# Performance work log

Measured on AMD Instinct MI355X. Metric: run time of the kernel, lower is better.

## Reference

```python
import jax, jax.numpy as jnp
import numpy as np

B, C, H, W = 8, 512, 64, 64
DEPTH, HEADS = 4, 8


def setup_inputs() -> dict:
    key = jax.random.key(0)
    ks = jax.random.split(key, 7)
    s = 0.02
    return {
        "x": jax.random.normal(ks[0], (B, C, H, W), jnp.float32),
        # axial positional embeddings, emb dim at index 1: (1,C,H,1) and (1,C,1,W)
        "pos_h": jax.random.normal(ks[1], (C, H), jnp.float32) * s,
        "pos_w": jax.random.normal(ks[2], (C, W), jnp.float32) * s,
        # per layer, per axis (0=height, 1=width): q, kv, out projections
        "wq": jax.random.normal(ks[3], (DEPTH, 2, C, C), jnp.float32) * s,
        "wkv": jax.random.normal(ks[4], (DEPTH, 2, C, 2 * C), jnp.float32) * s,
        "wo": jax.random.normal(ks[5], (DEPTH, 2, C, C), jnp.float32) * s,
        "wo_b": jax.random.normal(ks[6], (DEPTH, 2, C), jnp.float32) * s,
    }


def _attn_last_axis(x, wq, wkv, wo, wo_b, heads):
    """Self-attention along the second-to-last axis. x: (..., L, C)."""
    lead = x.shape[:-2]
    L, Cd = x.shape[-2], x.shape[-1]
    e = Cd // heads
    q = x @ wq                       # (..., L, C)
    k, v = jnp.split(x @ wkv, 2, axis=-1)
    sh = lead + (L, heads, e)
    q, k, v = q.reshape(sh), k.reshape(sh), v.reshape(sh)
    dots = jnp.einsum('...ihe,...jhe->...hij', q, k) * (e ** -0.5)
    attn = jax.nn.softmax(dots, axis=-1)
    out = jnp.einsum('...hij,...jhe->...ihe', attn, v).reshape(lead + (L, heads * e))
    return out @ wo + wo_b


def reference(x, pos_h, pos_w, wq, wkv, wo, wo_b):
    # positional embedding: x + (1,C,H,1) + (1,C,1,W)
    x = x + pos_h[None, :, :, None] + pos_w[None, :, None, :]
    y = jnp.transpose(x, (0, 2, 3, 1))  # (B,H,W,C) channels-last working layout
    for l in range(DEPTH):
        # height-axis attention: (B,W,H,C), attend along H
        yh = jnp.transpose(y, (0, 2, 1, 3))
        oh = _attn_last_axis(yh, wq[l, 0], wkv[l, 0], wo[l, 0], wo_b[l, 0], HEADS)
        oh = jnp.transpose(oh, (0, 2, 1, 3))
        # width-axis attention: attend along W
        ow = _attn_last_axis(y, wq[l, 1], wkv[l, 1], wo[l, 1], wo_b[l, 1], HEADS)
        y = oh + ow  # sum_axial_out=True, no residual
    return jnp.transpose(y, (0, 3, 1, 2))  # back to (B,C,H,W)
```

## Files before the change

kernel.cpp:

```cpp
#include <hip/hip_runtime.h>
#include <stdint.h>


typedef __attribute__((ext_vector_type(8))) short bf16x8;
typedef __attribute__((ext_vector_type(4))) float f32x4;
typedef unsigned short u16;
typedef unsigned int u32;

#define MFMA16(a, b, c) __builtin_amdgcn_mfma_f32_16x16x32_bf16((a), (b), (c), 0, 0, 0)

__device__ __forceinline__ float b2f(u16 h) {
    u32 u = ((u32)h) << 16;
    float f;
    __builtin_memcpy(&f, &u, 4);
    return f;
}
__device__ __forceinline__ u16 f2b(float f) {
    u32 u;
    __builtin_memcpy(&u, &f, 4);
    u32 r = (u + 0x7fffu + ((u >> 16) & 1u)) >> 16;
    return (u16)r;
}

#define GLD_LDS16(g, l)                                                        \
    __builtin_amdgcn_global_load_lds(                                          \
        (const __attribute__((address_space(1))) void*)(g),                    \
        (__attribute__((address_space(3))) void*)(l), 16, 0, 0)

__global__ __launch_bounds__(256) void embed_kernel(
    const float* __restrict__ x, const float* __restrict__ ph,
    const float* __restrict__ pw, u16* __restrict__ y)
{
    __shared__ float tile[64][65];
    const int c0 = blockIdx.x * 64, h = blockIdx.y, b = blockIdx.z;
    const int t = threadIdx.x;
#pragma unroll
    for (int i = 0; i < 4; ++i) {
        int cl = (t >> 4) + i * 16;
        int w4 = (t & 15) * 4;
        const float* src = x + (((size_t)(b * 512 + c0 + cl)) * 64 + h) * 64 + w4;
        float4 v = *(const float4*)src;
        float p = ph[(c0 + cl) * 64 + h];
        tile[cl][w4 + 0] = v.x + p + pw[(c0 + cl) * 64 + w4 + 0];
        tile[cl][w4 + 1] = v.y + p + pw[(c0 + cl) * 64 + w4 + 1];
        tile[cl][w4 + 2] = v.z + p + pw[(c0 + cl) * 64 + w4 + 2];
        tile[cl][w4 + 3] = v.w + p + pw[(c0 + cl) * 64 + w4 + 3];
    }
    __syncthreads();
    const int wl = t >> 2, cb = (t & 3) * 16;
    bf16x8 o0, o1;
#pragma unroll
    for (int j = 0; j < 8; ++j) o0[j] = (short)f2b(tile[cb + j][wl]);
#pragma unroll
    for (int j = 0; j < 8; ++j) o1[j] = (short)f2b(tile[cb + 8 + j][wl]);
    u16* dst = y + (((size_t)(b * 64 + h) * 64 + wl) * 512 + c0 + cb);
    *(bf16x8*)dst = o0;
    *(bf16x8*)(dst + 8) = o1;
}

__global__ __launch_bounds__(256) void wtrans_kernel(
    const float* __restrict__ wq, const float* __restrict__ wkv,
    const float* __restrict__ wo, u16* __restrict__ wT)
{
    const int mid = blockIdx.z;
    const int l = mid / 6, rest = mid % 6, axis = rest / 3, which = rest % 3;
    const size_t la = (size_t)(l * 2 + axis);
    const float* src;
    int N;
    size_t doff;
    if (which == 0)      { src = wq  + la * 512 * 512;  N = 512;  doff = la * (2048 * 512); }
    else if (which == 1) { src = wkv + la * 512 * 1024; N = 1024; doff = la * (2048 * 512) + 512 * 512; }
    else                 { src = wo  + la * 512 * 512;  N = 512;  doff = la * (2048 * 512) + 512 * 512 + 1024 * 512; }
    const int n0 = blockIdx.y * 64;
    if (n0 >= N) return;
    const int k0 = blockIdx.x * 64;
    __shared__ float tile[64][65];
    const int t = threadIdx.x;
#pragma unroll
    for (int i = 0; i < 4; ++i) {
        int kl = (t >> 4) + i * 16;
        int n4 = (t & 15) * 4;
        float4 v = *(const float4*)(src + (size_t)(k0 + kl) * N + n0 + n4);
        tile[kl][n4 + 0] = v.x; tile[kl][n4 + 1] = v.y;
        tile[kl][n4 + 2] = v.z; tile[kl][n4 + 3] = v.w;
    }
    __syncthreads();
    const int nl = t >> 2, kb = (t & 3) * 16;
    bf16x8 o0, o1;
#pragma unroll
    for (int j = 0; j < 8; ++j) o0[j] = (short)f2b(tile[kb + j][nl]);
#pragma unroll
    for (int j = 0; j < 8; ++j) o1[j] = (short)f2b(tile[kb + 8 + j][nl]);
    u16* dst = wT + doff + (size_t)(n0 + nl) * 512 + k0 + kb;
    *(bf16x8*)dst = o0;
    *(bf16x8*)(dst + 8) = o1;
}

template <int MODE>
__global__ __launch_bounds__(256) void gemm_bt(
    const u16* __restrict__ A, int lda,
    const u16* __restrict__ Bt,
    const float* __restrict__ bias,
    u16* C, int ldc)
{
    __shared__ u16 As[128 * 64];
    __shared__ u16 Bs[128 * 64];
    const int tid = threadIdx.x;
    const int lane = tid & 63;
    const int wv = tid >> 6;
    const int wr = (wv >> 1) * 64, wc = (wv & 1) * 64;
    const int nbx = gridDim.x;
    int lin = blockIdx.x + nbx * blockIdx.y;
    int cpx = (nbx * gridDim.y) >> 3;
    int id = (lin & 7) * cpx + (lin >> 3);
    const int n0 = (id % nbx) * 128;
    const int m0 = (id / nbx) * 128;
    const int rl = lane >> 3;
    const int cp = lane & 7;
    const int l16 = lane & 15;
    const int g = lane >> 4;
    const int kgrp = g << 3;
    f32x4 acc[4][4] = {};

    for (int ks = 0; ks < 512; ks += 64) {
#pragma unroll
        for (int i = 0; i < 4; ++i) {
            int row = wv * 8 + i * 32 + rl;
            int clog = cp ^ (row & 7);
            const u16* src = A + (size_t)(m0 + row) * lda + ks + clog * 8;
            GLD_LDS16(src, As + (wv * 8 + i * 32) * 64);
        }
#pragma unroll
        for (int i = 0; i < 4; ++i) {
            int row = wv * 8 + i * 32 + rl;
            int clog = cp ^ (row & 7);
            const u16* src = Bt + (size_t)(n0 + row) * 512 + ks + clog * 8;
            GLD_LDS16(src, Bs + (wv * 8 + i * 32) * 64);
        }
        __syncthreads();
#pragma unroll
        for (int kk = 0; kk < 2; ++kk) {
            bf16x8 af[4], bfr[4];
            const int kb = (kk * 32 + kgrp) * 2;
#pragma unroll
            for (int mf = 0; mf < 4; ++mf) {
                int row = wr + mf * 16 + l16;
                af[mf] = *(const bf16x8*)((const char*)As + row * 128 + (kb ^ ((row & 7) << 4)));
            }
#pragma unroll
            for (int nf = 0; nf < 4; ++nf) {
                int row = wc + nf * 16 + l16;
                bfr[nf] = *(const bf16x8*)((const char*)Bs + row * 128 + (kb ^ ((row & 7) << 4)));
            }
#pragma unroll
            for (int nf = 0; nf < 4; ++nf)
#pragma unroll
                for (int mf = 0; mf < 4; ++mf)
                    acc[nf][mf] = MFMA16(bfr[nf], af[mf], acc[nf][mf]);
        }
        __syncthreads();
    }

    float bv[4][4];
    if (MODE >= 1) {
#pragma unroll
        for (int nf = 0; nf < 4; ++nf) {
            float4 b4 = *(const float4*)(bias + n0 + wc + nf * 16 + g * 4);
            bv[nf][0] = b4.x; bv[nf][1] = b4.y; bv[nf][2] = b4.z; bv[nf][3] = b4.w;
        }
    }
#pragma unroll
    for (int mf = 0; mf < 4; ++mf) {
        const int m = m0 + wr + mf * 16 + l16;
#pragma unroll
        for (int nf = 0; nf < 4; ++nf) {
            const int n = n0 + wc + nf * 16 + g * 4;
            u16* cptr = C + (size_t)m * ldc + n;
            float v0 = acc[nf][mf][0], v1 = acc[nf][mf][1];
            float v2 = acc[nf][mf][2], v3 = acc[nf][mf][3];
            if (MODE >= 1) { v0 += bv[nf][0]; v1 += bv[nf][1]; v2 += bv[nf][2]; v3 += bv[nf][3]; }
            if (MODE == 2) {
                ushort4 o = *(const ushort4*)cptr;
                v0 += b2f(o.x); v1 += b2f(o.y); v2 += b2f(o.z); v3 += b2f(o.w);
            }
            uint2 pk;
            pk.x = (u32)f2b(v0) | ((u32)f2b(v1) << 16);
            pk.y = (u32)f2b(v2) | ((u32)f2b(v3) << 16);
            *(uint2*)cptr = pk;
        }
    }
}

__global__ __launch_bounds__(256) void attn_kernel(u16* QKV, int bstr, int tstr)
{
    __shared__ u16 sm[4][2][64 * 64];
    const int bi = blockIdx.x;
    const int base = (bi >> 6) * 4096 + (bi & 63) * bstr;
    const int tid = threadIdx.x, lane = tid & 63, wv = tid >> 6;
    const int l16 = lane & 15, g = lane >> 4;
    const int kgrp = g << 3;
    const int rl = lane >> 3, cp = lane & 7;
    u16* Kl = (u16*)sm[wv][0];
    u16* Vt = (u16*)sm[wv][1];

    for (int hh = 0; hh < 2; ++hh) {
        const int head = wv + hh * 4;
        const int hoff = head * 64;

#pragma unroll
        for (int i = 0; i < 8; ++i) {
            int row = i * 8 + rl;
            int clog = cp ^ (row & 7);
            const u16* src = QKV + (size_t)(base + row * tstr) * 1536 + 512 + hoff + clog * 8;
            GLD_LDS16(src, Kl + i * 8 * 64);
        }
        bf16x8 q[4][2];
#pragma unroll
        for (int i_f = 0; i_f < 4; ++i_f)
#pragma unroll
            for (int k2 = 0; k2 < 2; ++k2)
                q[i_f][k2] = *(const bf16x8*)(QKV + (size_t)(base + (i_f * 16 + l16) * tstr) * 1536
                                              + hoff + k2 * 32 + kgrp);
        bf16x8 vvr[8];
#pragma unroll
        for (int i = 0; i < 8; ++i)
            vvr[i] = *(const bf16x8*)(QKV + (size_t)(base + (i * 8 + rl) * tstr) * 1536
                                      + 1024 + hoff + cp * 8);

        asm volatile("s_waitcnt vmcnt(0)" ::: "memory");
        __builtin_amdgcn_sched_barrier(0);

        f32x4 st[4][4] = {};
#pragma unroll
        for (int k2 = 0; k2 < 2; ++k2) {
            bf16x8 kf[4];
            const int kb = (k2 * 32 + kgrp) * 2;
#pragma unroll
            for (int j_f = 0; j_f < 4; ++j_f) {
                int row = j_f * 16 + l16;
                kf[j_f] = *(const bf16x8*)((const char*)Kl + row * 128 + (kb ^ ((row & 7) << 4)));
            }
#pragma unroll
            for (int i_f = 0; i_f < 4; ++i_f)
#pragma unroll
                for (int j_f = 0; j_f < 4; ++j_f)
                    st[i_f][j_f] = MFMA16(kf[j_f], q[i_f][k2], st[i_f][j_f]);
        }

#pragma unroll
        for (int i = 0; i < 8; ++i) {
            int j2 = i * 16 + rl * 2;
#pragma unroll
            for (int t = 0; t < 8; ++t) {
                int e = cp * 8 + t;
                int addr = e * 128 + (j2 ^ (((t ^ cp) & 7) << 4));
                *(u16*)((char*)Vt + addr) = (u16)vvr[i][t];
            }
        }

#pragma unroll
        for (int i_f = 0; i_f < 4; ++i_f) {
            const int irow = i_f * 16 + l16;
            float ev[4][4];
            float mx = -1e30f;
#pragma unroll
            for (int j_f = 0; j_f < 4; ++j_f)
#pragma unroll
                for (int r = 0; r < 4; ++r) {
                    float v = st[i_f][j_f][r] * 0.125f;
                    ev[j_f][r] = v;
                    mx = fmaxf(mx, v);
                }
            mx = fmaxf(mx, __shfl_xor(mx, 16, 64));
            mx = fmaxf(mx, __shfl_xor(mx, 32, 64));
            float sum = 0.f;
#pragma unroll
            for (int j_f = 0; j_f < 4; ++j_f)
#pragma unroll
                for (int r = 0; r < 4; ++r) {
                    float e = __expf(ev[j_f][r] - mx);
                    ev[j_f][r] = e;
                    sum += e;
                }
            sum += __shfl_xor(sum, 16, 64);
            sum += __shfl_xor(sum, 32, 64);
            float inv = __builtin_amdgcn_rcpf(sum);
#pragma unroll
            for (int j_f = 0; j_f < 4; ++j_f) {
                uint2 pk;
                pk.x = (u32)f2b(ev[j_f][0] * inv) | ((u32)f2b(ev[j_f][1] * inv) << 16);
                pk.y = (u32)f2b(ev[j_f][2] * inv) | ((u32)f2b(ev[j_f][3] * inv) << 16);
                int addr = irow * 128 + ((j_f * 32 + g * 8) ^ ((irow & 7) << 4));
                *(uint2*)((char*)Kl + addr) = pk;
            }
        }

        f32x4 of[4][4] = {};
#pragma unroll
        for (int k2 = 0; k2 < 2; ++k2) {
            bf16x8 vf[4], pf[4];
            const int kb = (k2 * 32 + kgrp) * 2;
#pragma unroll
            for (int e_f = 0; e_f < 4; ++e_f) {
                int row = e_f * 16 + l16;
                int sw = ((row & 7) ^ ((row >> 3) & 7)) << 4;
                vf[e_f] = *(const bf16x8*)((const char*)Vt + row * 128 + (kb ^ sw));
            }
#pragma unroll
            for (int i_f = 0; i_f < 4; ++i_f) {
                int row = i_f * 16 + l16;
                pf[i_f] = *(const bf16x8*)((const char*)Kl + row * 128 + (kb ^ ((row & 7) << 4)));
            }
#pragma unroll
            for (int e_f = 0; e_f < 4; ++e_f)
#pragma unroll
                for (int i_f = 0; i_f < 4; ++i_f)
                    of[e_f][i_f] = MFMA16(vf[e_f], pf[i_f], of[e_f][i_f]);
        }

#pragma unroll
        for (int i_f = 0; i_f < 4; ++i_f) {
            const int i = i_f * 16 + l16;
            u16* orow = QKV + (size_t)(base + i * tstr) * 1536 + hoff + g * 4;
#pragma unroll
            for (int e_f = 0; e_f < 4; ++e_f) {
                uint2 pk;
                pk.x = (u32)f2b(of[e_f][i_f][0]) | ((u32)f2b(of[e_f][i_f][1]) << 16);
                pk.y = (u32)f2b(of[e_f][i_f][2]) | ((u32)f2b(of[e_f][i_f][3]) << 16);
                *(uint2*)(orow + e_f * 16) = pk;
            }
        }
        asm volatile("s_waitcnt lgkmcnt(0)" ::: "memory");
        __builtin_amdgcn_sched_barrier(0);
    }
}

__global__ __launch_bounds__(256) void untrans_kernel(
    const u16* __restrict__ y, float* __restrict__ out)
{
    __shared__ float tile[64][65];
    const int c0 = blockIdx.x * 64, h = blockIdx.y, b = blockIdx.z;
    const int t = threadIdx.x;
    {
        const int wl = t >> 2, cb = (t & 3) * 16;
        const u16* src = y + (((size_t)(b * 64 + h) * 64 + wl) * 512 + c0 + cb);
        bf16x8 v0 = *(const bf16x8*)src;
        bf16x8 v1 = *(const bf16x8*)(src + 8);
#pragma unroll
        for (int j = 0; j < 8; ++j) tile[wl][cb + j] = b2f((u16)v0[j]);
#pragma unroll
        for (int j = 0; j < 8; ++j) tile[wl][cb + 8 + j] = b2f((u16)v1[j]);
    }
    __syncthreads();
    const int cl = t >> 2, w16 = (t & 3) * 16;
    float* dst = out + (((size_t)(b * 512 + c0 + cl)) * 64 + h) * 64 + w16;
#pragma unroll
    for (int j = 0; j < 4; ++j) {
        float4 v;
        v.x = tile[w16 + j * 4 + 0][cl];
        v.y = tile[w16 + j * 4 + 1][cl];
        v.z = tile[w16 + j * 4 + 2][cl];
        v.w = tile[w16 + j * 4 + 3][cl];
        *(float4*)(dst + j * 4) = v;
    }
}

extern "C" void kernel_launch(void* const* d_in, const int* in_sizes, int n_in,
                              void* d_out, int out_size, void* d_ws, size_t ws_size,
                              hipStream_t stream)
{
    (void)in_sizes; (void)n_in; (void)out_size; (void)ws_size;
    const float* x   = (const float*)d_in[0];
    const float* ph  = (const float*)d_in[1];
    const float* pw  = (const float*)d_in[2];
    const float* wq  = (const float*)d_in[3];
    const float* wkv = (const float*)d_in[4];
    const float* wo  = (const float*)d_in[5];
    const float* wob = (const float*)d_in[6];

    char* ws = (char*)d_ws;
    u16* yA  = (u16*)(ws);
    u16* yB  = (u16*)(ws + 33554432);
    u16* QKV = (u16*)(ws + 67108864);
    u16* wT  = (u16*)(ws + 167772160);
    float* out = (float*)d_out;

    embed_kernel<<<dim3(8, 64, 8), 256, 0, stream>>>(x, ph, pw, yA);
    wtrans_kernel<<<dim3(8, 16, 24), 256, 0, stream>>>(wq, wkv, wo, wT);

    u16* yin = yA;
    u16* yout = yB;
    for (int l = 0; l < 4; ++l) {
        for (int axis = 0; axis < 2; ++axis) {
            const u16* wTla = wT + (size_t)(l * 2 + axis) * 2048 * 512;
            const float* bias = wob + (size_t)(l * 2 + axis) * 512;
            gemm_bt<0><<<dim3(12, 256), 256, 0, stream>>>(yin, 512, wTla, nullptr, QKV, 1536);
            int bstr = (axis == 0) ? 1 : 64;
            int tstr = (axis == 0) ? 64 : 1;
            attn_kernel<<<dim3(512), 256, 0, stream>>>(QKV, bstr, tstr);
            const u16* woT = wTla + 512 * 512 + 1024 * 512;
            if (axis == 0)
                gemm_bt<1><<<dim3(4, 256), 256, 0, stream>>>(QKV, 1536, woT, bias, yout, 512);
            else
                gemm_bt<2><<<dim3(4, 256), 256, 0, stream>>>(QKV, 1536, woT, bias, yout, 512);
        }
        u16* tmp = yin; yin = yout; yout = tmp;
    }
    untrans_kernel<<<dim3(8, 64, 8), 256, 0, stream>>>(yin, out);
}
```

Before: 1.233 ms.

## Store height-axis QKV transposed so attention reads contiguous rows, one head per wave

The QKV GEMM epilogue for the height axis now writes rows in permuted order (swapping h and w within each batch), so the attention kernel always reads contiguous sequence rows instead of strided ones. The out-projection GEMM uses the same inverse permutation when writing y. The attention kernel drops its two-head loop and strided addressing, assigning one (sequence, head) unit per wave and doubling the grid. This removes the 64-row stride for height attention and adds occupancy, at the cost of scattered row writes in the GEMM epilogues.

```diff
diff --git a/kernel.cpp b/kernel.cpp
--- a/kernel.cpp
+++ b/kernel.cpp
@@ -96,7 +96,7 @@
     *(bf16x8*)(dst + 8) = o1;
 }
 
-template <int MODE>
+template <int MODE, int PERM>
 __global__ __launch_bounds__(256) void gemm_bt(
     const u16* __restrict__ A, int lda,
     const u16* __restrict__ Bt,
@@ -172,10 +172,12 @@
 #pragma unroll
     for (int mf = 0; mf < 4; ++mf) {
         const int m = m0 + wr + mf * 16 + l16;
+        const int mp = PERM ? ((m & ~4095) | ((m & 63) << 6) | ((m >> 6) & 63)) : m;
+        u16* crow = C + (size_t)mp * ldc;
 #pragma unroll
         for (int nf = 0; nf < 4; ++nf) {
             const int n = n0 + wc + nf * 16 + g * 4;
-            u16* cptr = C + (size_t)m * ldc + n;
+            u16* cptr = crow + n;
             float v0 = acc[nf][mf][0], v1 = acc[nf][mf][1];
             float v2 = acc[nf][mf][2], v3 = acc[nf][mf][3];
             if (MODE >= 1) { v0 += bv[nf][0]; v1 += bv[nf][1]; v2 += bv[nf][2]; v3 += bv[nf][3]; }
@@ -191,147 +193,141 @@
     }
 }
 
-__global__ __launch_bounds__(256) void attn_kernel(u16* QKV, int bstr, int tstr)
+__global__ __launch_bounds__(256) void attn_kernel(u16* QKV)
 {
     __shared__ u16 sm[4][2][64 * 64];
-    const int bi = blockIdx.x;
-    const int base = (bi >> 6) * 4096 + (bi & 63) * bstr;
     const int tid = threadIdx.x, lane = tid & 63, wv = tid >> 6;
+    const int unit = blockIdx.x * 4 + wv;
+    const int base = (unit >> 3) * 64;
+    const int hoff = (unit & 7) * 64;
     const int l16 = lane & 15, g = lane >> 4;
     const int kgrp = g << 3;
     const int rl = lane >> 3, cp = lane & 7;
     u16* Kl = (u16*)sm[wv][0];
     u16* Vt = (u16*)sm[wv][1];
 
-    for (int hh = 0; hh < 2; ++hh) {
-        const int head = wv + hh * 4;
-        const int hoff = head * 64;
-
-#pragma unroll
-        for (int i = 0; i < 8; ++i) {
-            int row = i * 8 + rl;
-            int clog = cp ^ (row & 7);
-            const u16* src = QKV + (size_t)(base + row * tstr) * 1536 + 512 + hoff + clog * 8;
-            GLD_LDS16(src, Kl + i * 8 * 64);
-        }
-        bf16x8 q[4][2];
+#pragma unroll
+    for (int i = 0; i < 8; ++i) {
+        int row = i * 8 + rl;
+        int clog = cp ^ (row & 7);
+        const u16* src = QKV + (size_t)(base + row) * 1536 + 512 + hoff + clog * 8;
+        GLD_LDS16(src, Kl + i * 8 * 64);
+    }
+    bf16x8 q[4][2];
+#pragma unroll
+    for (int i_f = 0; i_f < 4; ++i_f)
+#pragma unroll
+        for (int k2 = 0; k2 < 2; ++k2)
+            q[i_f][k2] = *(const bf16x8*)(QKV + (size_t)(base + i_f * 16 + l16) * 1536
+                                          + hoff + k2 * 32 + kgrp);
+    bf16x8 vvr[8];
+#pragma unroll
+    for (int i = 0; i < 8; ++i)
+        vvr[i] = *(const bf16x8*)(QKV + (size_t)(base + i * 8 + rl) * 1536
+                                  + 1024 + hoff + cp * 8);
+
+    asm volatile("s_waitcnt vmcnt(0)" ::: "memory");
+    __builtin_amdgcn_sched_barrier(0);
+
+    f32x4 st[4][4] = {};
+#pragma unroll
+    for (int k2 = 0; k2 < 2; ++k2) {
+        bf16x8 kf[4];
+        const int kb = (k2 * 32 + kgrp) * 2;
+#pragma unroll
+        for (int j_f = 0; j_f < 4; ++j_f) {
+            int row = j_f * 16 + l16;
+            kf[j_f] = *(const bf16x8*)((const char*)Kl + row * 128 + (kb ^ ((row & 7) << 4)));
+        }
 #pragma unroll
         for (int i_f = 0; i_f < 4; ++i_f)
 #pragma unroll
-            for (int k2 = 0; k2 < 2; ++k2)
-                q[i_f][k2] = *(const bf16x8*)(QKV + (size_t)(base + (i_f * 16 + l16) * tstr) * 1536
-                                              + hoff + k2 * 32 + kgrp);
-        bf16x8 vvr[8];
-#pragma unroll
-        for (int i = 0; i < 8; ++i)
-            vvr[i] = *(const bf16x8*)(QKV + (size_t)(base + (i * 8 + rl) * tstr) * 1536
-                                      + 1024 + hoff + cp * 8);
-
-        asm volatile("s_waitcnt vmcnt(0)" ::: "memory");
-        __builtin_amdgcn_sched_barrier(0);
-
-        f32x4 st[4][4] = {};
-#pragma unroll
-        for (int k2 = 0; k2 < 2; ++k2) {
-            bf16x8 kf[4];
-            const int kb = (k2 * 32 + kgrp) * 2;
-#pragma unroll
-            for (int j_f = 0; j_f < 4; ++j_f) {
-                int row = j_f * 16 + l16;
-                kf[j_f] = *(const bf16x8*)((const char*)Kl + row * 128 + (kb ^ ((row & 7) << 4)));
+            for (int j_f = 0; j_f < 4; ++j_f)
+                st[i_f][j_f] = MFMA16(kf[j_f], q[i_f][k2], st[i_f][j_f]);
+    }
+
+#pragma unroll
+    for (int i = 0; i < 8; ++i) {
+        int j2 = i * 16 + rl * 2;
+#pragma unroll
+        for (int t = 0; t < 8; ++t) {
+            int e = cp * 8 + t;
+            int addr = e * 128 + (j2 ^ (((t ^ cp) & 7) << 4));
+            *(u16*)((char*)Vt + addr) = (u16)vvr[i][t];
+        }
+    }
+
+#pragma unroll
+    for (int i_f = 0; i_f < 4; ++i_f) {
+        const int irow = i_f * 16 + l16;
+        float ev[4][4];
+        float mx = -1e30f;
+#pragma unroll
+        for (int j_f = 0; j_f < 4; ++j_f)
+#pragma unroll
+            for (int r = 0; r < 4; ++r) {
+                float v = st[i_f][j_f][r] * 0.125f;
+                ev[j_f][r] = v;
+                mx = fmaxf(mx, v);
             }
+        mx = fmaxf(mx, __shfl_xor(mx, 16, 64));
+        mx = fmaxf(mx, __shfl_xor(mx, 32, 64));
+        float sum = 0.f;
+#pragma unroll
+        for (int j_f = 0; j_f < 4; ++j_f)
+#pragma unroll
+            for (int r = 0; r < 4; ++r) {
+                float e = __expf(ev[j_f][r] - mx);
+                ev[j_f][r] = e;
+                sum += e;
+            }
+        sum += __shfl_xor(sum, 16, 64);
+        sum += __shfl_xor(sum, 32, 64);
+        float inv = __builtin_amdgcn_rcpf(sum);
+#pragma unroll
+        for (int j_f = 0; j_f < 4; ++j_f) {
+            uint2 pk;
+            pk.x = (u32)f2b(ev[j_f][0] * inv) | ((u32)f2b(ev[j_f][1] * inv) << 16);
+            pk.y = (u32)f2b(ev[j_f][2] * inv) | ((u32)f2b(ev[j_f][3] * inv) << 16);
+            int addr = irow * 128 + ((j_f * 32 + g * 8) ^ ((irow & 7) << 4));
+            *(uint2*)((char*)Kl + addr) = pk;
+        }
+    }
+
+    f32x4 of[4][4] = {};
+#pragma unroll
+    for (int k2 = 0; k2 < 2; ++k2) {
+        bf16x8 vf[4], pf[4];
+        const int kb = (k2 * 32 + kgrp) * 2;
+#pragma unroll
+        for (int e_f = 0; e_f < 4; ++e_f) {
+            int row = e_f * 16 + l16;
+            int sw = ((row & 7) ^ ((row >> 3) & 7)) << 4;
+            vf[e_f] = *(const bf16x8*)((const char*)Vt + row * 128 + (kb ^ sw));
+        }
+#pragma unroll
+        for (int i_f = 0; i_f < 4; ++i_f) {
+            int row = i_f * 16 + l16;
+            pf[i_f] = *(const bf16x8*)((const char*)Kl + row * 128 + (kb ^ ((row & 7) << 4)));
+        }
+#pragma unroll
+        for (int e_f = 0; e_f < 4; ++e_f)
 #pragma unroll
             for (int i_f = 0; i_f < 4; ++i_f)
-#pragma unroll
-                for (int j_f = 0; j_f < 4; ++j_f)
-                    st[i_f][j_f] = MFMA16(kf[j_f], q[i_f][k2], st[i_f][j_f]);
-        }
-
-#pragma unroll
-        for (int i = 0; i < 8; ++i) {
-            int j2 = i * 16 + rl * 2;
-#pragma unroll
-            for (int t = 0; t < 8; ++t) {
-                int e = cp * 8 + t;
-                int addr = e * 128 + (j2 ^ (((t ^ cp) & 7) << 4));
-                *(u16*)((char*)Vt + addr) = (u16)vvr[i][t];
-            }
-        }
-
-#pragma unroll
-        for (int i_f = 0; i_f < 4; ++i_f) {
-            const int irow = i_f * 16 + l16;
-            float ev[4][4];
-            float mx = -1e30f;
-#pragma unroll
-            for (int j_f = 0; j_f < 4; ++j_f)
-#pragma unroll
-                for (int r = 0; r < 4; ++r) {
-                    float v = st[i_f][j_f][r] * 0.125f;
-                    ev[j_f][r] = v;
-                    mx = fmaxf(mx, v);
-                }
-            mx = fmaxf(mx, __shfl_xor(mx, 16, 64));
-            mx = fmaxf(mx, __shfl_xor(mx, 32, 64));
-            float sum = 0.f;
-#pragma unroll
-            for (int j_f = 0; j_f < 4; ++j_f)
-#pragma unroll
-                for (int r = 0; r < 4; ++r) {
-                    float e = __expf(ev[j_f][r] - mx);
-                    ev[j_f][r] = e;
-                    sum += e;
-                }
-            sum += __shfl_xor(sum, 16, 64);
-            sum += __shfl_xor(sum, 32, 64);
-            float inv = __builtin_amdgcn_rcpf(sum);
-#pragma unroll
-            for (int j_f = 0; j_f < 4; ++j_f) {
-                uint2 pk;
-                pk.x = (u32)f2b(ev[j_f][0] * inv) | ((u32)f2b(ev[j_f][1] * inv) << 16);
-                pk.y = (u32)f2b(ev[j_f][2] * inv) | ((u32)f2b(ev[j_f][3] * inv) << 16);
-                int addr = irow * 128 + ((j_f * 32 + g * 8) ^ ((irow & 7) << 4));
-                *(uint2*)((char*)Kl + addr) = pk;
-            }
-        }
-
-        f32x4 of[4][4] = {};
-#pragma unroll
-        for (int k2 = 0; k2 < 2; ++k2) {
-            bf16x8 vf[4], pf[4];
-            const int kb = (k2 * 32 + kgrp) * 2;
-#pragma unroll
-            for (int e_f = 0; e_f < 4; ++e_f) {
-                int row = e_f * 16 + l16;
-                int sw = ((row & 7) ^ ((row >> 3) & 7)) << 4;
-                vf[e_f] = *(const bf16x8*)((const char*)Vt + row * 128 + (kb ^ sw));
-            }
-#pragma unroll
-            for (int i_f = 0; i_f < 4; ++i_f) {
-                int row = i_f * 16 + l16;
-                pf[i_f] = *(const bf16x8*)((const char*)Kl + row * 128 + (kb ^ ((row & 7) << 4)));
-            }
-#pragma unroll
-            for (int e_f = 0; e_f < 4; ++e_f)
-#pragma unroll
-                for (int i_f = 0; i_f < 4; ++i_f)
-                    of[e_f][i_f] = MFMA16(vf[e_f], pf[i_f], of[e_f][i_f]);
-        }
-
-#pragma unroll
-        for (int i_f = 0; i_f < 4; ++i_f) {
-            const int i = i_f * 16 + l16;
-            u16* orow = QKV + (size_t)(base + i * tstr) * 1536 + hoff + g * 4;
-#pragma unroll
-            for (int e_f = 0; e_f < 4; ++e_f) {
-                uint2 pk;
-                pk.x = (u32)f2b(of[e_f][i_f][0]) | ((u32)f2b(of[e_f][i_f][1]) << 16);
-                pk.y = (u32)f2b(of[e_f][i_f][2]) | ((u32)f2b(of[e_f][i_f][3]) << 16);
-                *(uint2*)(orow + e_f * 16) = pk;
-            }
-        }
-        asm volatile("s_waitcnt lgkmcnt(0)" ::: "memory");
-        __builtin_amdgcn_sched_barrier(0);
+                of[e_f][i_f] = MFMA16(vf[e_f], pf[i_f], of[e_f][i_f]);
+    }
+
+#pragma unroll
+    for (int i_f = 0; i_f < 4; ++i_f) {
+        const int i = i_f * 16 + l16;
+        u16* orow = QKV + (size_t)(base + i) * 1536 + hoff + g * 4;
+#pragma unroll
+        for (int e_f = 0; e_f < 4; ++e_f) {
+            uint2 pk;
+            pk.x = (u32)f2b(of[e_f][i_f][0]) | ((u32)f2b(of[e_f][i_f][1]) << 16);
+            pk.y = (u32)f2b(of[e_f][i_f][2]) | ((u32)f2b(of[e_f][i_f][3]) << 16);
+            *(uint2*)(orow + e_f * 16) = pk;
+        }
     }
 }
 
@@ -394,15 +390,16 @@
         for (int axis = 0; axis < 2; ++axis) {
             const u16* wTla = wT + (size_t)(l * 2 + axis) * 2048 * 512;
             const float* bias = wob + (size_t)(l * 2 + axis) * 512;
-            gemm_bt<0><<<dim3(12, 256), 256, 0, stream>>>(yin, 512, wTla, nullptr, QKV, 1536);
-            int bstr = (axis == 0) ? 1 : 64;
-            int tstr = (axis == 0) ? 64 : 1;
-            attn_kernel<<<dim3(512), 256, 0, stream>>>(QKV, bstr, tstr);
             const u16* woT = wTla + 512 * 512 + 1024 * 512;
             if (axis == 0)
-                gemm_bt<1><<<dim3(4, 256), 256, 0, stream>>>(QKV, 1536, woT, bias, yout, 512);
+                gemm_bt<0, 1><<<dim3(12, 256), 256, 0, stream>>>(yin, 512, wTla, nullptr, QKV, 1536);
             else
-                gemm_bt<2><<<dim3(4, 256), 256, 0, stream>>>(QKV, 1536, woT, bias, yout, 512);
+                gemm_bt<0, 0><<<dim3(12, 256), 256, 0, stream>>>(yin, 512, wTla, nullptr, QKV, 1536);
+            attn_kernel<<<dim3(1024), 256, 0, stream>>>(QKV);
+            if (axis == 0)
+                gemm_bt<1, 1><<<dim3(4, 256), 256, 0, stream>>>(QKV, 1536, woT, bias, yout, 512);
+            else
+                gemm_bt<2, 0><<<dim3(4, 256), 256, 0, stream>>>(QKV, 1536, woT, bias, yout, 512);
         }
         u16* tmp = yin; yin = yout; yout = tmp;
     }
```

After: 1.181 ms. -4.2%, faster.
